# Kernel tuning notes

Measured on AMD Instinct MI355X. Metric: run time of the kernel, lower is better.

The kernel has to match this reference:

```python
import jax, jax.numpy as jnp
import numpy as np

N_NODES = 50000
N_EDGES = 1000000
N_GRAPHS = 256
ORIG = 92
ATOM = 64
NBR = 41
EPS = 1e-5


def _bn_train(h, gamma, beta):
    # BatchNorm1d in training mode: batch stats, biased variance
    mu = h.mean(axis=0)
    var = jnp.var(h, axis=0)
    return (h - mu) * jax.lax.rsqrt(var + EPS) * gamma + beta


def setup_inputs() -> dict:
    key = jax.random.key(0)
    ks = jax.random.split(key, 16)
    inp = {
        "x": jax.random.normal(ks[0], (N_NODES, ORIG), dtype=jnp.float32),
        "edge_attr": jax.random.normal(ks[1], (N_EDGES, NBR), dtype=jnp.float32),
        "lower_f": jax.random.normal(ks[2], (N_NODES, ATOM), dtype=jnp.float32),
        "edge_index": jax.random.randint(ks[3], (2, N_EDGES), 0, N_NODES, dtype=jnp.int32),
        "batch": jnp.sort(jax.random.randint(ks[4], (N_NODES,), 0, N_GRAPHS, dtype=jnp.int32)),
        # params
        "emb_W": jax.random.normal(ks[5], (ORIG, ATOM), dtype=jnp.float32) / np.sqrt(ORIG),
        "emb_b": jnp.zeros((ATOM,), dtype=jnp.float32),
        "fc_W": jax.random.normal(ks[6], (2 * ATOM + NBR, 2 * ATOM), dtype=jnp.float32) / np.sqrt(2 * ATOM + NBR),
        "fc_b": jnp.zeros((2 * ATOM,), dtype=jnp.float32),
        "bn1_g": jnp.ones((2 * ATOM,), dtype=jnp.float32),
        "bn1_b": jnp.zeros((2 * ATOM,), dtype=jnp.float32),
        "bn2_g": jnp.ones((ATOM,), dtype=jnp.float32),
        "bn2_b": jnp.zeros((ATOM,), dtype=jnp.float32),
        "att_W": jax.random.normal(ks[7], (ATOM, 1), dtype=jnp.float32) / np.sqrt(ATOM),
        "att_b": jnp.zeros((1,), dtype=jnp.float32),
        "out_W": jax.random.normal(ks[8], (ATOM, 1), dtype=jnp.float32) / np.sqrt(ATOM),
        "out_b": jnp.zeros((1,), dtype=jnp.float32),
    }
    return inp


def reference(x, edge_attr, lower_f, emb_W, emb_b, fc_W, fc_b, bn1_g, bn1_b,
              bn2_g, bn2_b, att_W, att_b, out_W, out_b, edge_index, batch):
    # embedding + lower-level features
    atom_fea = x @ emb_W + emb_b + lower_f  # [N, ATOM]

    # CGConv: gather endpoints, concat with edge features
    src, dst = edge_index[0], edge_index[1]
    total = jnp.concatenate([atom_fea[src], atom_fea[dst], edge_attr], axis=-1)  # [E, 2A+NBR]
    gated = _bn_train(total @ fc_W + fc_b, bn1_g, bn1_b)  # [E, 2A]
    nbr_filter, nbr_core = gated[:, :ATOM], gated[:, ATOM:]
    msg = jax.nn.sigmoid(nbr_filter) * jax.nn.softplus(nbr_core)  # [E, A]
    summed = jax.ops.segment_sum(msg, src, num_segments=N_NODES)  # [N, A]
    atom_out = _bn_train(summed, bn2_g, bn2_b)

    # SiLU + attentional aggregation per graph
    h = jax.nn.silu(atom_out)  # [N, A]
    logits = (h @ att_W + att_b)[:, 0]  # [N]
    seg_max = jax.ops.segment_max(logits, batch, num_segments=N_GRAPHS)
    e = jnp.exp(logits - seg_max[batch])
    denom = jax.ops.segment_sum(e, batch, num_segments=N_GRAPHS)
    alpha = e / denom[batch]  # [N]
    crys = jax.ops.segment_sum(alpha[:, None] * h, batch, num_segments=N_GRAPHS)  # [G, A]
    crys_fea = crys @ out_W + out_b  # [G, 1]
    return atom_out, crys_fea
```

## Files before the change

kernel.cpp:

```cpp
#include <hip/hip_runtime.h>
#include <math.h>

#define NN 50000
#define NE 1000000
#define NG 256
#define ORIGD 92
#define NBRD 41
#define NSPREAD 32
#define SCAN_B 256

typedef unsigned short u16;
typedef __attribute__((ext_vector_type(8))) short short8;
typedef __attribute__((ext_vector_type(4))) float f32x4;
typedef __attribute__((ext_vector_type(8))) float f32x8;

#define OFF_AFB     0
#define OFF_SUMMED  1600000
#define OFF_WT      4800000
#define OFF_BN1SPR  4812288
#define OFF_BN1SC   4820480
#define OFF_BN2ACC  4820736
#define OFF_BN2SC   4820864
#define OFF_ELOG    4820992
#define OFF_SEGMAX  4870992
#define OFF_DENOM   4871248
#define OFF_CNT     4871504
#define OFF_PTR     4921504
#define OFF_HEAD    4971504
#define OFF_BSUM    5021504
#define OFF_BOFS    5021760
#define OFF_EIDX    5022016
#define OFF_H       6022016
#define OFF_T2_END  70022016
#define OFF_P       70022016
#define OFF_T3_END  82822016
#define OFF_SRCC    82822016
#define OFF_DSTC    83822016
#define OFF_EAB     84822016
#define OFF_T4_END  108822016

__device__ __forceinline__ u16 f2b(float f) {
    unsigned u = __float_as_uint(f);
    return (u16)((u + 0x7FFFu + ((u >> 16) & 1u)) >> 16);
}
__device__ __forceinline__ float b2f(u16 u) {
    return __uint_as_float(((unsigned)u) << 16);
}
__device__ __forceinline__ float gate(float f, float cc) {
    float sig = __builtin_amdgcn_rcpf(1.f + __expf(-f));
    float sp  = fmaxf(cc, 0.f) + __logf(1.f + __expf(-fabsf(cc)));
    return sig * sp;
}
__device__ __forceinline__ float fsilu(float x) {
    return x * __builtin_amdgcn_rcpf(1.f + __expf(-x));
}

__global__ __launch_bounds__(256) void k_embed2(
    const float* __restrict__ x, const float* __restrict__ lf,
    const float* __restrict__ W, const float* __restrict__ b,
    u16* __restrict__ afb, const float* __restrict__ fcW,
    u16* __restrict__ wT3, u16* __restrict__ wP, float* __restrict__ ws)
{
    int gid = blockIdx.x * 256 + threadIdx.x;
    int n = gid >> 6, c = gid & 63;
    const float* xr = x + (long)n * ORIGD;
    float acc = b[c] + lf[gid];
#pragma unroll 4
    for (int k = 0; k < ORIGD; k++)
        acc = fmaf(xr[k], W[k * 64 + c], acc);
    afb[gid] = f2b(acc);

    if (blockIdx.x < 96) {
        int i = blockIdx.x * 256 + threadIdx.x;
        if (i < 8192) {
            int j = i >> 6, k = i & 63;
            wT3[i] = (k < NBRD) ? f2b(fcW[(128 + k) * 128 + j]) : (u16)0;
        } else {
            int i2 = i - 8192;
            int j = i2 >> 6, k = i2 & 63;
            int row = (j < 128) ? k : (64 + k);
            wP[i2] = f2b(fcW[row * 128 + (j & 127)]);
        }
    } else if (blockIdx.x < 336) {
        int zid = (blockIdx.x - 96) * 256 + threadIdx.x;
        if (zid < 8704) {
            ws[OFF_BN1SPR + zid] = 0.f;
        } else {
            int z2 = zid - 8704;
            if (z2 < 50512) ws[OFF_SEGMAX + z2] = 0.f;
        }
    }
}

__global__ void k_prepw(const float* __restrict__ fcW, u16* __restrict__ wT)
{
    int i = blockIdx.x * 256 + threadIdx.x;
    int j = i / 192, k = i - j * 192;
    wT[i] = (k < 169) ? f2b(fcW[k * 128 + j]) : (u16)0;
}

__global__ void k_prepw2(const float* __restrict__ fcW, u16* __restrict__ wT3,
                         u16* __restrict__ wP)
{
    int i = blockIdx.x * 256 + threadIdx.x;
    if (i < 8192) {
        int j = i >> 6, k = i & 63;
        wT3[i] = (k < NBRD) ? f2b(fcW[(128 + k) * 128 + j]) : (u16)0;
    } else {
        int i2 = i - 8192;
        int j = i2 >> 6, k = i2 & 63;
        int row = (j < 128) ? k : (64 + k);
        wP[i2] = f2b(fcW[row * 128 + (j & 127)]);
    }
}

__global__ __launch_bounds__(256) void k_embed(
    const float* __restrict__ x, const float* __restrict__ lf,
    const float* __restrict__ W, const float* __restrict__ b,
    u16* __restrict__ afb)
{
    int gid = blockIdx.x * 256 + threadIdx.x;
    int n = gid >> 6, c = gid & 63;
    const float* xr = x + (long)n * ORIGD;
    float acc = b[c] + lf[gid];
#pragma unroll 4
    for (int k = 0; k < ORIGD; k++)
        acc = fmaf(xr[k], W[k * 64 + c], acc);
    afb[gid] = f2b(acc);
}

template <int PACKED>
__global__ __launch_bounds__(256) void k_pnode(
    const u16* __restrict__ afb, const u16* __restrict__ wP, float* __restrict__ P)
{
    __shared__ __align__(16) u16 sB[64 * 72];
    const int tid = threadIdx.x;
    const int n0 = blockIdx.x * 64;

    for (int i = tid; i < 512; i += 256) {
        int r = i >> 3, c = i & 7;
        int n = n0 + r;
        short8 v = {0,0,0,0,0,0,0,0};
        if (n < NN) v = *(const short8*)(afb + (long)n * 64 + c * 8);
        *(short8*)(sB + r * 72 + c * 8) = v;
    }
    __syncthreads();

    const int lane = tid & 63, w = tid >> 6;
    const int n16 = lane & 15, quad = lane >> 4;
    short8 A[4][2];
#pragma unroll
    for (int m = 0; m < 4; m++) {
        const u16* base = wP + (16 * (w + 4 * m) + n16) * 64 + quad * 8;
        A[m][0] = *(const short8*)(base);
        A[m][1] = *(const short8*)(base + 32);
    }
    for (int t = 0; t < 4; t++) {
        const u16* row = sB + (16 * t + n16) * 72 + quad * 8;
        short8 b0 = *(const short8*)(row);
        short8 b1 = *(const short8*)(row + 32);
        int n = n0 + 16 * t + n16;
#pragma unroll
        for (int m = 0; m < 4; m++) {
            f32x4 acc = {0.f, 0.f, 0.f, 0.f};
            acc = __builtin_amdgcn_mfma_f32_16x16x32_bf16(A[m][0], b0, acc, 0, 0, 0);
            acc = __builtin_amdgcn_mfma_f32_16x16x32_bf16(A[m][1], b1, acc, 0, 0, 0);
            if (n < NN) {
                int M = w + 4 * m;
                int j;
                if (PACKED) {
                    int MM = M & 7;
                    j = ((M >> 3) * 128) + ((MM & 3) * 4 + quad) * 8 + ((MM >> 2) << 2);
                } else {
                    j = 16 * M + 4 * quad;
                }
                *(f32x4*)(P + (long)n * 256 + j) = acc;
            }
        }
    }
}

__global__ void k_hist(const int* __restrict__ ei, int* __restrict__ cnt)
{
    int e = blockIdx.x * 256 + threadIdx.x;
    if (e < NE) atomicAdd(&cnt[ei[e]], 1);
}

__global__ __launch_bounds__(256) void k_hist2(
    const int* __restrict__ ei, const float* __restrict__ ea,
    int* __restrict__ cnt, u16* __restrict__ eaB)
{
    long gid = (long)blockIdx.x * 256 + threadIdx.x;
    if (gid >= (long)NE * 6) return;
    int e = (int)(gid / 6);
    int q = (int)(gid - (long)e * 6);
    if (q == 0) atomicAdd(&cnt[ei[e]], 1);
    const float* row = ea + (long)e * NBRD;
    int c0 = q * 8;
    short8 v;
#pragma unroll
    for (int j = 0; j < 8; j++) {
        int c = c0 + j;
        v[j] = (c < NBRD) ? (short)f2b(row[c]) : (short)0;
    }
    *(short8*)(eaB + (long)e * 48 + c0) = v;
}

__global__ void k_partial(const int* __restrict__ cnt, int* __restrict__ lofs,
                          int* __restrict__ bsum)
{
    __shared__ int sd[SCAN_B];
    int t = threadIdx.x, b = blockIdx.x, n = b * SCAN_B + t;
    int v = (n < NN) ? cnt[n] : 0;
    sd[t] = v; __syncthreads();
    for (int o = 1; o < SCAN_B; o <<= 1) {
        int x = (t >= o) ? sd[t - o] : 0;
        __syncthreads();
        sd[t] += x;
        __syncthreads();
    }
    if (n < NN) lofs[n] = sd[t] - v;
    if (t == SCAN_B - 1) bsum[b] = sd[t];
}

__global__ void k_scanb(const int* __restrict__ bsum, int* __restrict__ bofs, int nb)
{
    __shared__ int sd[256];
    int t = threadIdx.x;
    int v = (t < nb) ? bsum[t] : 0;
    sd[t] = v; __syncthreads();
    for (int o = 1; o < 256; o <<= 1) {
        int x = (t >= o) ? sd[t - o] : 0;
        __syncthreads();
        sd[t] += x;
        __syncthreads();
    }
    bofs[t] = sd[t] - v;
}

__global__ void k_addofs(int* __restrict__ ptr, const int* __restrict__ bofs,
                         int* __restrict__ head)
{
    int n = blockIdx.x * 256 + threadIdx.x;
    if (n < NN) {
        int p = ptr[n] + bofs[n >> 8];
        ptr[n] = p; head[n] = p;
    }
}

__global__ void k_fill(const int* __restrict__ ei, int* __restrict__ head,
                       int* __restrict__ eidx)
{
    int e = blockIdx.x * 256 + threadIdx.x;
    if (e < NE) {
        int pos = atomicAdd(&head[ei[e]], 1);
        eidx[pos] = e;
    }
}

__global__ void k_fill2(const int* __restrict__ ei, int* __restrict__ head,
                        int* __restrict__ eidx, int* __restrict__ srcC,
                        int* __restrict__ dstC)
{
    int e = blockIdx.x * 256 + threadIdx.x;
    if (e < NE) {
        int s = ei[e];
        int pos = atomicAdd(&head[s], 1);
        eidx[pos] = e;
        srcC[pos] = s;
        dstC[pos] = ei[NE + e];
    }
}

__global__ __launch_bounds__(256, 4) void k_gemm_h5(
    const u16* __restrict__ eaB, const int* __restrict__ eidx,
    const int* __restrict__ srcC, const int* __restrict__ dstC,
    const u16* __restrict__ wT3, const float* __restrict__ P,
    u16* __restrict__ h, float* __restrict__ spread)
{
    const int tid = threadIdx.x;
    const int e0 = blockIdx.x * 64;
    const int lane = tid & 63, w = tid >> 6;
    const int n16 = lane & 15, quad = lane >> 4;

    short8 A0[2], A1[2];
    {
        const u16* a0 = wT3 + (16 * w + n16) * 64 + quad * 8;
        const u16* a1 = wT3 + (16 * (w + 4) + n16) * 64 + quad * 8;
        A0[0] = *(const short8*)(a0);  A0[1] = *(const short8*)(a0 + 32);
        A1[0] = *(const short8*)(a1);  A1[1] = *(const short8*)(a1 + 32);
    }

    const int j0 = 16 * w + 4 * quad;
    const int pofs = (w * 4 + quad) * 8;
    const short8 bz = {0,0,0,0,0,0,0,0};
    float s0[4] = {0,0,0,0}, q0[4] = {0,0,0,0}, s1[4] = {0,0,0,0}, q1[4] = {0,0,0,0};

    short8 b0A, b1A, b0B, b1B;
    f32x8 gSA, gDA, gSB, gDB;

#define LOADT(t, b0v, b1v, gSv, gDv)                                       \
    {                                                                      \
        int p_ = e0 + 16 * (t) + n16;                                      \
        int s_ = srcC[p_], d_ = dstC[p_], e_ = eidx[p_];                   \
        const u16* er_ = eaB + (long)e_ * 48;                              \
        b0v = *(const short8*)(er_ + quad * 8);                            \
        b1v = (quad < 2) ? *(const short8*)(er_ + 32 + quad * 8) : bz;     \
        gSv = *(const f32x8*)(P + (long)s_ * 256 + pofs);                  \
        gDv = *(const f32x8*)(P + (long)d_ * 256 + 128 + pofs);            \
    }

#define COMPT(t, b0v, b1v, gSv, gDv)                                       \
    {                                                                      \
        f32x4 acc0 = {0.f,0.f,0.f,0.f}, acc1 = {0.f,0.f,0.f,0.f};          \
        acc0 = __builtin_amdgcn_mfma_f32_16x16x32_bf16(A0[0], b0v, acc0, 0, 0, 0); \
        acc0 = __builtin_amdgcn_mfma_f32_16x16x32_bf16(A0[1], b1v, acc0, 0, 0, 0); \
        acc1 = __builtin_amdgcn_mfma_f32_16x16x32_bf16(A1[0], b0v, acc1, 0, 0, 0); \
        acc1 = __builtin_amdgcn_mfma_f32_16x16x32_bf16(A1[1], b1v, acc1, 0, 0, 0); \
        u16 hv0[4], hv1[4];                                                \
        _Pragma("unroll")                                                  \
        for (int r = 0; r < 4; r++) {                                      \
            float u0 = acc0[r] + gSv[r] + gDv[r];                          \
            float u1 = acc1[r] + gSv[4 + r] + gDv[4 + r];                  \
            s0[r] += u0; q0[r] = fmaf(u0, u0, q0[r]);                      \
            s1[r] += u1; q1[r] = fmaf(u1, u1, q1[r]);                      \
            hv0[r] = f2b(u0); hv1[r] = f2b(u1);                            \
        }                                                                  \
        u16* hp = h + (long)(e0 + 16 * (t) + n16) * 128 + j0;              \
        ushort4 v0 = make_ushort4(hv0[0], hv0[1], hv0[2], hv0[3]);         \
        ushort4 v1 = make_ushort4(hv1[0], hv1[1], hv1[2], hv1[3]);         \
        *(ushort4*)hp = v0;                                                \
        *(ushort4*)(hp + 64) = v1;                                         \
    }

    LOADT(0, b0A, b1A, gSA, gDA);
    LOADT(1, b0B, b1B, gSB, gDB);
    COMPT(0, b0A, b1A, gSA, gDA);
    LOADT(2, b0A, b1A, gSA, gDA);
    COMPT(1, b0B, b1B, gSB, gDB);
    LOADT(3, b0B, b1B, gSB, gDB);
    COMPT(2, b0A, b1A, gSA, gDA);
    COMPT(3, b0B, b1B, gSB, gDB);

#undef LOADT
#undef COMPT

#pragma unroll
    for (int m = 1; m < 16; m <<= 1) {
#pragma unroll
        for (int r = 0; r < 4; r++) {
            s0[r] += __shfl_xor(s0[r], m); q0[r] += __shfl_xor(q0[r], m);
            s1[r] += __shfl_xor(s1[r], m); q1[r] += __shfl_xor(q1[r], m);
        }
    }
    if (n16 == 0) {
        float* sp = spread + (blockIdx.x & (NSPREAD - 1)) * 256;
#pragma unroll
        for (int r = 0; r < 4; r++) {
            atomicAdd(sp + j0 + r,       s0[r]);
            atomicAdd(sp + 128 + j0 + r, q0[r]);
            atomicAdd(sp + 64 + j0 + r,  s1[r]);
            atomicAdd(sp + 192 + j0 + r, q1[r]);
        }
    }
}

__global__ __launch_bounds__(256) void k_gemm_h2(
    const float* __restrict__ ea, const int* __restrict__ ei,
    const u16* __restrict__ wT3, const float* __restrict__ P,
    u16* __restrict__ h, float* __restrict__ spread)
{
    __shared__ __align__(16) u16 sTl[64 * 72];
    __shared__ int sSrc[64], sDst[64];
    const int tid = threadIdx.x;
    const int e0 = blockIdx.x * 64;

    if (tid < 64) sSrc[tid] = ei[e0 + tid];
    else if (tid < 128) sDst[tid - 64] = ei[NE + e0 + tid - 64];

    for (int i = tid; i < 64 * 64; i += 256) {
        int e = i >> 6, c = i & 63;
        float v = (c < NBRD) ? ea[(long)(e0 + e) * NBRD + c] : 0.f;
        sTl[e * 72 + c] = f2b(v);
    }
    __syncthreads();

    const int lane = tid & 63, w = tid >> 6;
    const int n16 = lane & 15, quad = lane >> 4;

    short8 A0[2], A1[2];
    {
        const u16* b0 = wT3 + (16 * w + n16) * 64 + quad * 8;
        const u16* b1 = wT3 + (16 * (w + 4) + n16) * 64 + quad * 8;
        A0[0] = *(const short8*)(b0);  A0[1] = *(const short8*)(b0 + 32);
        A1[0] = *(const short8*)(b1);  A1[1] = *(const short8*)(b1 + 32);
    }

    const int j0 = 16 * w + 4 * quad;
    float s0[4] = {0,0,0,0}, q0[4] = {0,0,0,0}, s1[4] = {0,0,0,0}, q1[4] = {0,0,0,0};

    for (int t = 0; t < 4; t++) {
        const int ge16 = 16 * t + n16;
        const int src = sSrc[ge16], dst = sDst[ge16];
        const float* pS = P + (long)src * 256;
        const float* pD = P + (long)dst * 256 + 128;
        f32x4 g0 = *(const f32x4*)(pS + j0);
        f32x4 g1 = *(const f32x4*)(pS + 64 + j0);
        f32x4 g2 = *(const f32x4*)(pD + j0);
        f32x4 g3 = *(const f32x4*)(pD + 64 + j0);

        const u16* row = sTl + ge16 * 72 + quad * 8;
        short8 b0 = *(const short8*)(row);
        short8 b1 = *(const short8*)(row + 32);
        f32x4 acc0 = {0.f, 0.f, 0.f, 0.f}, acc1 = {0.f, 0.f, 0.f, 0.f};
        acc0 = __builtin_amdgcn_mfma_f32_16x16x32_bf16(A0[0], b0, acc0, 0, 0, 0);
        acc0 = __builtin_amdgcn_mfma_f32_16x16x32_bf16(A0[1], b1, acc0, 0, 0, 0);
        acc1 = __builtin_amdgcn_mfma_f32_16x16x32_bf16(A1[0], b0, acc1, 0, 0, 0);
        acc1 = __builtin_amdgcn_mfma_f32_16x16x32_bf16(A1[1], b1, acc1, 0, 0, 0);

        u16 hv0[4], hv1[4];
#pragma unroll
        for (int r = 0; r < 4; r++) {
            float u0 = acc0[r] + g0[r] + g2[r];
            float u1 = acc1[r] + g1[r] + g3[r];
            s0[r] += u0; q0[r] = fmaf(u0, u0, q0[r]);
            s1[r] += u1; q1[r] = fmaf(u1, u1, q1[r]);
            hv0[r] = f2b(u0); hv1[r] = f2b(u1);
        }
        int ge = e0 + ge16;
        u16* hp = h + (long)ge * 128 + j0;
        ushort4 v0 = make_ushort4(hv0[0], hv0[1], hv0[2], hv0[3]);
        ushort4 v1 = make_ushort4(hv1[0], hv1[1], hv1[2], hv1[3]);
        *(ushort4*)hp = v0;
        *(ushort4*)(hp + 64) = v1;
    }

#pragma unroll
    for (int m = 1; m < 16; m <<= 1) {
#pragma unroll
        for (int r = 0; r < 4; r++) {
            s0[r] += __shfl_xor(s0[r], m); q0[r] += __shfl_xor(q0[r], m);
            s1[r] += __shfl_xor(s1[r], m); q1[r] += __shfl_xor(q1[r], m);
        }
    }
    if (n16 == 0) {
        float* sp = spread + (blockIdx.x & (NSPREAD - 1)) * 256;
#pragma unroll
        for (int r = 0; r < 4; r++) {
            atomicAdd(sp + j0 + r,       s0[r]);
            atomicAdd(sp + 128 + j0 + r, q0[r]);
            atomicAdd(sp + 64 + j0 + r,  s1[r]);
            atomicAdd(sp + 192 + j0 + r, q1[r]);
        }
    }
}

__global__ __launch_bounds__(256) void k_gemm_h(
    const u16* __restrict__ afb, const float* __restrict__ ea,
    const int* __restrict__ ei, const u16* __restrict__ wT,
    u16* __restrict__ h, float* __restrict__ spread)
{
    __shared__ __align__(16) u16 sTl[64 * 200];
    __shared__ int sSrc[64], sDst[64];
    const int tid = threadIdx.x;
    const int e0 = blockIdx.x * 64;

    if (tid < 64) sSrc[tid] = ei[e0 + tid];
    else if (tid < 128) sDst[tid - 64] = ei[NE + e0 + tid - 64];
    __syncthreads();

    for (int i = tid; i < 1024; i += 256) {
        int e = i >> 4, q = i & 15;
        const u16* g = (q < 8) ? (afb + (long)sSrc[e] * 64 + q * 8)
                               : (afb + (long)sDst[e] * 64 + (q - 8) * 8);
        *(short8*)(sTl + e * 200 + q * 8) = *(const short8*)g;
    }
    for (int i = tid; i < 64 * 64; i += 256) {
        int e = i >> 6, c = i & 63;
        float v = (c < NBRD) ? ea[(long)(e0 + e) * NBRD + c] : 0.f;
        sTl[e * 200 + 128 + c] = f2b(v);
    }
    __syncthreads();

    const int lane = tid & 63, w = tid >> 6;
    const int n16 = lane & 15, quad = lane >> 4;

    short8 A0[6], A1[6];
    {
        const u16* b0 = wT + (16 * w + n16) * 192 + quad * 8;
        const u16* b1 = wT + (16 * (w + 4) + n16) * 192 + quad * 8;
#pragma unroll
        for (int ks = 0; ks < 6; ks++) {
            A0[ks] = *(const short8*)(b0 + ks * 32);
            A1[ks] = *(const short8*)(b1 + ks * 32);
        }
    }

    const int j0 = 16 * w + 4 * quad;
    float s0[4] = {0,0,0,0}, q0[4] = {0,0,0,0}, s1[4] = {0,0,0,0}, q1[4] = {0,0,0,0};

    for (int t = 0; t < 4; t++) {
        const u16* row = sTl + (16 * t + n16) * 200 + quad * 8;
        f32x4 acc0 = {0.f, 0.f, 0.f, 0.f}, acc1 = {0.f, 0.f, 0.f, 0.f};
#pragma unroll
        for (int ks = 0; ks < 6; ks++) {
            short8 b = *(const short8*)(row + ks * 32);
            acc0 = __builtin_amdgcn_mfma_f32_16x16x32_bf16(A0[ks], b, acc0, 0, 0, 0);
            acc1 = __builtin_amdgcn_mfma_f32_16x16x32_bf16(A1[ks], b, acc1, 0, 0, 0);
        }
#pragma unroll
        for (int r = 0; r < 4; r++) {
            s0[r] += acc0[r]; q0[r] = fmaf(acc0[r], acc0[r], q0[r]);
            s1[r] += acc1[r]; q1[r] = fmaf(acc1[r], acc1[r], q1[r]);
        }
        int ge = e0 + 16 * t + n16;
        u16* hp = h + (long)ge * 128 + j0;
        ushort4 v0 = make_ushort4(f2b(acc0[0]), f2b(acc0[1]), f2b(acc0[2]), f2b(acc0[3]));
        ushort4 v1 = make_ushort4(f2b(acc1[0]), f2b(acc1[1]), f2b(acc1[2]), f2b(acc1[3]));
        *(ushort4*)hp = v0;
        *(ushort4*)(hp + 64) = v1;
    }

#pragma unroll
    for (int m = 1; m < 16; m <<= 1) {
#pragma unroll
        for (int r = 0; r < 4; r++) {
            s0[r] += __shfl_xor(s0[r], m); q0[r] += __shfl_xor(q0[r], m);
            s1[r] += __shfl_xor(s1[r], m); q1[r] += __shfl_xor(q1[r], m);
        }
    }
    if (n16 == 0) {
        float* sp = spread + (blockIdx.x & (NSPREAD - 1)) * 256;
#pragma unroll
        for (int r = 0; r < 4; r++) {
            atomicAdd(sp + j0 + r,       s0[r]);
            atomicAdd(sp + 128 + j0 + r, q0[r]);
            atomicAdd(sp + 64 + j0 + r,  s1[r]);
            atomicAdd(sp + 192 + j0 + r, q1[r]);
        }
    }
}

template <int MODE>
__global__ __launch_bounds__(256) void k_gemm(
    const u16* __restrict__ afb, const float* __restrict__ ea,
    const int* __restrict__ ei, const u16* __restrict__ wT,
    const float* __restrict__ sc, float* __restrict__ outbuf)
{
    __shared__ __align__(16) u16 sTl[64 * 200];
    __shared__ int sSrc[64], sDst[64];
    const int tid = threadIdx.x;
    const int e0 = blockIdx.x * 64;

    if (tid < 64) sSrc[tid] = ei[e0 + tid];
    else if (tid < 128) sDst[tid - 64] = ei[NE + e0 + tid - 64];
    __syncthreads();
    for (int i = tid; i < 1024; i += 256) {
        int e = i >> 4, q = i & 15;
        const u16* g = (q < 8) ? (afb + (long)sSrc[e] * 64 + q * 8)
                               : (afb + (long)sDst[e] * 64 + (q - 8) * 8);
        *(short8*)(sTl + e * 200 + q * 8) = *(const short8*)g;
    }
    for (int i = tid; i < 64 * 64; i += 256) {
        int e = i >> 6, c = i & 63;
        float v = (c < NBRD) ? ea[(long)(e0 + e) * NBRD + c] : 0.f;
        sTl[e * 200 + 128 + c] = f2b(v);
    }
    __syncthreads();

    const int lane = tid & 63, w = tid >> 6;
    const int n16 = lane & 15, quad = lane >> 4;
    short8 A0[6], A1[6];
    {
        const u16* b0 = wT + (16 * w + n16) * 192 + quad * 8;
        const u16* b1 = wT + (16 * (w + 4) + n16) * 192 + quad * 8;
#pragma unroll
        for (int ks = 0; ks < 6; ks++) {
            A0[ks] = *(const short8*)(b0 + ks * 32);
            A1[ks] = *(const short8*)(b1 + ks * 32);
        }
    }
    const int j0 = 16 * w + 4 * quad;
    float s0[4] = {0,0,0,0}, q0[4] = {0,0,0,0}, s1[4] = {0,0,0,0}, q1[4] = {0,0,0,0};
    float scf[4], shf[4], scc[4], shc[4];
    if (MODE == 1) {
#pragma unroll
        for (int r = 0; r < 4; r++) {
            scf[r] = sc[j0 + r];        shf[r] = sc[128 + j0 + r];
            scc[r] = sc[64 + j0 + r];   shc[r] = sc[192 + j0 + r];
        }
    }
    for (int t = 0; t < 4; t++) {
        const u16* row = sTl + (16 * t + n16) * 200 + quad * 8;
        f32x4 acc0 = {0.f, 0.f, 0.f, 0.f}, acc1 = {0.f, 0.f, 0.f, 0.f};
#pragma unroll
        for (int ks = 0; ks < 6; ks++) {
            short8 b = *(const short8*)(row + ks * 32);
            acc0 = __builtin_amdgcn_mfma_f32_16x16x32_bf16(A0[ks], b, acc0, 0, 0, 0);
            acc1 = __builtin_amdgcn_mfma_f32_16x16x32_bf16(A1[ks], b, acc1, 0, 0, 0);
        }
        if (MODE == 0) {
#pragma unroll
            for (int r = 0; r < 4; r++) {
                s0[r] += acc0[r]; q0[r] = fmaf(acc0[r], acc0[r], q0[r]);
                s1[r] += acc1[r]; q1[r] = fmaf(acc1[r], acc1[r], q1[r]);
            }
        } else {
            int src = sSrc[16 * t + n16];
            float* dst = outbuf + (long)src * 64 + j0;
#pragma unroll
            for (int r = 0; r < 4; r++) {
                float f  = fmaf(acc0[r], scf[r], shf[r]);
                float cc = fmaf(acc1[r], scc[r], shc[r]);
                atomicAdd(dst + r, gate(f, cc));
            }
        }
    }
    if (MODE == 0) {
#pragma unroll
        for (int m = 1; m < 16; m <<= 1) {
#pragma unroll
            for (int r = 0; r < 4; r++) {
                s0[r] += __shfl_xor(s0[r], m); q0[r] += __shfl_xor(q0[r], m);
                s1[r] += __shfl_xor(s1[r], m); q1[r] += __shfl_xor(q1[r], m);
            }
        }
        if (n16 == 0) {
            float* sp = outbuf + (blockIdx.x & (NSPREAD - 1)) * 256;
#pragma unroll
            for (int r = 0; r < 4; r++) {
                atomicAdd(sp + j0 + r,       s0[r]);
                atomicAdd(sp + 128 + j0 + r, q0[r]);
                atomicAdd(sp + 64 + j0 + r,  s1[r]);
                atomicAdd(sp + 192 + j0 + r, q1[r]);
            }
        }
    }
}

__global__ void k_bn1fin(const float* __restrict__ spread,
                         const float* __restrict__ g, const float* __restrict__ b,
                         float* __restrict__ sc)
{
    int c = threadIdx.x;
    float s = 0.f, q = 0.f;
    for (int k = 0; k < NSPREAD; k++) { s += spread[k * 256 + c]; q += spread[k * 256 + 128 + c]; }
    float mean_acc = s / (float)NE;
    float var = q / (float)NE - mean_acc * mean_acc;
    float scale = g[c] * rsqrtf(var + 1e-5f);
    sc[c] = scale;
    sc[128 + c] = b[c] - mean_acc * scale;
}

__global__ __launch_bounds__(256) void k_scatter3(
    const u16* __restrict__ h, const int* __restrict__ ptr,
    const int* __restrict__ cnt, const float* __restrict__ spread,
    const float* __restrict__ g, const float* __restrict__ b,
    float* __restrict__ summed)
{
    __shared__ float ssc[256];
    int tid = threadIdx.x;
    if (tid < 128) {
        int c = tid;
        float s = 0.f, q = 0.f;
        for (int k = 0; k < NSPREAD; k++) {
            s += spread[k * 256 + c]; q += spread[k * 256 + 128 + c];
        }
        float mean_acc = s / (float)NE;
        float var = q / (float)NE - mean_acc * mean_acc;
        float scale = g[c] * rsqrtf(var + 1e-5f);
        ssc[c] = scale;
        ssc[128 + c] = b[c] - mean_acc * scale;
    }
    __syncthreads();

    int n = blockIdx.x * 4 + (tid >> 6);
    int l = tid & 63;
    int es = l & 7, cg = l >> 3;

    float scf[8], shf[8], scc[8], shc[8];
#pragma unroll
    for (int j = 0; j < 8; j++) {
        scf[j] = ssc[cg * 8 + j];
        shf[j] = ssc[128 + cg * 8 + j];
        scc[j] = ssc[64 + cg * 8 + j];
        shc[j] = ssc[192 + cg * 8 + j];
    }

    int p0 = ptr[n], deg = cnt[n];
    float acc[8] = {0,0,0,0,0,0,0,0};
    for (int i = 0; i < deg; i += 8) {
        int idx = i + es;
        bool valid = idx < deg;
        int row = p0 + (valid ? idx : 0);
        const u16* hr = h + (long)row * 128;
        short8 f8 = *(const short8*)(hr + cg * 8);
        short8 c8 = *(const short8*)(hr + 64 + cg * 8);
#pragma unroll
        for (int j = 0; j < 8; j++) {
            float f  = fmaf(b2f((u16)f8[j]), scf[j], shf[j]);
            float cc = fmaf(b2f((u16)c8[j]), scc[j], shc[j]);
            float gg = gate(f, cc);
            acc[j] += valid ? gg : 0.f;
        }
    }
#pragma unroll
    for (int m = 1; m < 8; m <<= 1)
#pragma unroll
        for (int j = 0; j < 8; j++) acc[j] += __shfl_xor(acc[j], m);
    if (es == 0) {
        float* sp = summed + (long)n * 64 + cg * 8;
        float4 v0 = {acc[0], acc[1], acc[2], acc[3]};
        float4 v1 = {acc[4], acc[5], acc[6], acc[7]};
        *(float4*)sp = v0;
        *(float4*)(sp + 4) = v1;
    }
}

__global__ __launch_bounds__(256) void k_scatter(
    const u16* __restrict__ h, const int* __restrict__ ptr,
    const int* __restrict__ cnt, const int* __restrict__ eidx,
    const float* __restrict__ sc, float* __restrict__ summed)
{
    int tid = threadIdx.x;
    int n = blockIdx.x * 4 + (tid >> 6);
    int l = tid & 63;
    int es = l & 7, cg = l >> 3;

    float4 a0 = *(const float4*)(sc + cg * 8);
    float4 a1 = *(const float4*)(sc + cg * 8 + 4);
    float4 b0 = *(const float4*)(sc + 128 + cg * 8);
    float4 b1 = *(const float4*)(sc + 128 + cg * 8 + 4);
    float4 c0 = *(const float4*)(sc + 64 + cg * 8);
    float4 c1 = *(const float4*)(sc + 64 + cg * 8 + 4);
    float4 d0 = *(const float4*)(sc + 192 + cg * 8);
    float4 d1 = *(const float4*)(sc + 192 + cg * 8 + 4);
    float scf[8] = {a0.x,a0.y,a0.z,a0.w,a1.x,a1.y,a1.z,a1.w};
    float shf[8] = {b0.x,b0.y,b0.z,b0.w,b1.x,b1.y,b1.z,b1.w};
    float scc[8] = {c0.x,c0.y,c0.z,c0.w,c1.x,c1.y,c1.z,c1.w};
    float shc[8] = {d0.x,d0.y,d0.z,d0.w,d1.x,d1.y,d1.z,d1.w};

    int p0 = ptr[n], deg = cnt[n];
    float acc[8] = {0,0,0,0,0,0,0,0};
    for (int i = 0; i < deg; i += 8) {
        int idx = i + es;
        bool valid = idx < deg;
        int e = eidx[p0 + (valid ? idx : 0)];
        const u16* hr = h + (long)e * 128;
        short8 f8 = *(const short8*)(hr + cg * 8);
        short8 c8 = *(const short8*)(hr + 64 + cg * 8);
#pragma unroll
        for (int j = 0; j < 8; j++) {
            float f  = fmaf(b2f((u16)f8[j]), scf[j], shf[j]);
            float cc = fmaf(b2f((u16)c8[j]), scc[j], shc[j]);
            float gg = gate(f, cc);
            acc[j] += valid ? gg : 0.f;
        }
    }
#pragma unroll
    for (int m = 1; m < 8; m <<= 1)
#pragma unroll
        for (int j = 0; j < 8; j++) acc[j] += __shfl_xor(acc[j], m);
    if (es == 0) {
        float* sp = summed + (long)n * 64 + cg * 8;
        float4 v0 = {acc[0], acc[1], acc[2], acc[3]};
        float4 v1 = {acc[4], acc[5], acc[6], acc[7]};
        *(float4*)sp = v0;
        *(float4*)(sp + 4) = v1;
    }
}

__global__ __launch_bounds__(256) void k_bn2stats(const float* __restrict__ summed,
                                                  float* __restrict__ acc2)
{
    int tid = threadIdx.x; int c = tid & 63; int sub = tid >> 6;
    float s = 0.f, q = 0.f;
    for (int r = blockIdx.x * 4 + sub; r < NN; r += 4 * 128) {
        float v = summed[(long)r * 64 + c]; s += v; q = fmaf(v, v, q);
    }
    __shared__ float rs[256], rq[256];
    rs[tid] = s; rq[tid] = q; __syncthreads();
    if (tid < 64) {
        s = rs[tid] + rs[tid + 64] + rs[tid + 128] + rs[tid + 192];
        q = rq[tid] + rq[tid + 64] + rq[tid + 128] + rq[tid + 192];
        atomicAdd(&acc2[tid], s);
        atomicAdd(&acc2[64 + tid], q);
    }
}

__global__ void k_bn2fin(const float* __restrict__ acc2,
                         const float* __restrict__ g, const float* __restrict__ b,
                         float* __restrict__ sc2, const float* __restrict__ outb,
                         float* __restrict__ out)
{
    int c = threadIdx.x;
    if (c < 64) {
        float mean = acc2[c] / (float)NN;
        float var = acc2[64 + c] / (float)NN - mean * mean;
        float scale = g[c] * rsqrtf(var + 1e-5f);
        sc2[c] = scale;
        sc2[64 + c] = b[c] - mean * scale;
    }
    out[(long)NN * 64 + c] = outb[0];
}

__global__ __launch_bounds__(256) void k_nodepost2(
    const float* __restrict__ summed, const float* __restrict__ acc2,
    const float* __restrict__ g, const float* __restrict__ b,
    const float* __restrict__ attW, const float* __restrict__ attb,
    const int* __restrict__ batch, float* __restrict__ out,
    float* __restrict__ elog, unsigned* __restrict__ segmax)
{
    __shared__ float ssc2[128];
    int tid = threadIdx.x;
    if (tid < 64) {
        float mean = acc2[tid] / (float)NN;
        float var = acc2[64 + tid] / (float)NN - mean * mean;
        float scale = g[tid] * rsqrtf(var + 1e-5f);
        ssc2[tid] = scale;
        ssc2[64 + tid] = b[tid] - mean * scale;
    }
    __syncthreads();

    int n = blockIdx.x * 4 + (tid >> 6); int c = tid & 63;
    float v = summed[(long)n * 64 + c];
    float ao = fmaf(v, ssc2[c], ssc2[64 + c]);
    out[(long)n * 64 + c] = ao;
    float h = fsilu(ao);
    float p = h * attW[c];
#pragma unroll
    for (int off = 32; off; off >>= 1) p += __shfl_down(p, off, 64);
    if (c == 0) {
        float logit = p + attb[0];
        elog[n] = logit;
        unsigned u = __float_as_uint(logit);
        u = (u & 0x80000000u) ? ~u : (u | 0x80000000u);
        atomicMax(&segmax[batch[n]], u);
    }
}

__global__ __launch_bounds__(256) void k_nodepost(
    const float* __restrict__ summed, const float* __restrict__ sc2,
    const float* __restrict__ attW, const float* __restrict__ attb,
    const int* __restrict__ batch, float* __restrict__ out,
    float* __restrict__ elog, unsigned* __restrict__ segmax)
{
    int tid = threadIdx.x; int n = blockIdx.x * 4 + (tid >> 6); int c = tid & 63;
    float v = summed[(long)n * 64 + c];
    float ao = fmaf(v, sc2[c], sc2[64 + c]);
    out[(long)n * 64 + c] = ao;
    float h = fsilu(ao);
    float p = h * attW[c];
#pragma unroll
    for (int off = 32; off; off >>= 1) p += __shfl_down(p, off, 64);
    if (c == 0) {
        float logit = p + attb[0];
        elog[n] = logit;
        unsigned u = __float_as_uint(logit);
        u = (u & 0x80000000u) ? ~u : (u | 0x80000000u);
        atomicMax(&segmax[batch[n]], u);
    }
}

__global__ void k_denom2(const int* __restrict__ batch,
                         const unsigned* __restrict__ segmax,
                         float* __restrict__ elog, float* __restrict__ denom,
                         const float* __restrict__ outb, float* __restrict__ out)
{
    int n = blockIdx.x * 256 + threadIdx.x;
    if (n < NG) out[(long)NN * 64 + n] = outb[0];
    if (n >= NN) return;
    int b = batch[n];
    unsigned u = segmax[b];
    u = (u & 0x80000000u) ? (u & 0x7FFFFFFFu) : ~u;
    float e = __expf(elog[n] - __uint_as_float(u));
    elog[n] = e;
    atomicAdd(&denom[b], e);
}

__global__ void k_denom(const int* __restrict__ batch,
                        const unsigned* __restrict__ segmax,
                        float* __restrict__ elog, float* __restrict__ denom)
{
    int n = blockIdx.x * 256 + threadIdx.x;
    if (n >= NN) return;
    int b = batch[n];
    unsigned u = segmax[b];
    u = (u & 0x80000000u) ? (u & 0x7FFFFFFFu) : ~u;
    float e = __expf(elog[n] - __uint_as_float(u));
    elog[n] = e;
    atomicAdd(&denom[b], e);
}

__global__ __launch_bounds__(256) void k_crys(
    const float* __restrict__ atom_out, const float* __restrict__ elog,
    const float* __restrict__ denom, const int* __restrict__ batch,
    const float* __restrict__ outW, float* __restrict__ out)
{
    int tid = threadIdx.x; int n = blockIdx.x * 4 + (tid >> 6); int l = tid & 63;
    int b = batch[n];
    float alpha = elog[n] / denom[b];
    float ao = atom_out[(long)n * 64 + l];
    float p = fsilu(ao) * outW[l];
#pragma unroll
    for (int off = 32; off; off >>= 1) p += __shfl_down(p, off, 64);
    if (l == 0) atomicAdd(&out[(long)NN * 64 + b], alpha * p);
}

extern "C" void kernel_launch(void* const* d_in, const int* in_sizes, int n_in,
                              void* d_out, int out_size, void* d_ws, size_t ws_size,
                              hipStream_t stream)
{
    const float* x    = (const float*)d_in[0];
    const float* eatt = (const float*)d_in[1];
    const float* lf   = (const float*)d_in[2];
    const int*   ei   = (const int*)d_in[3];
    const int*   batch= (const int*)d_in[4];
    const float* embW = (const float*)d_in[5];
    const float* embB = (const float*)d_in[6];
    const float* fcW  = (const float*)d_in[7];
    const float* bn1g = (const float*)d_in[9];
    const float* bn1b = (const float*)d_in[10];
    const float* bn2g = (const float*)d_in[11];
    const float* bn2b = (const float*)d_in[12];
    const float* attW = (const float*)d_in[13];
    const float* attB = (const float*)d_in[14];
    const float* outW = (const float*)d_in[15];
    const float* outB = (const float*)d_in[16];
    float* out = (float*)d_out;
    float* ws  = (float*)d_ws;

    u16* afb  = (u16*)(ws + OFF_AFB);
    u16* wT   = (u16*)(ws + OFF_WT);
    int* cnt  = (int*)(ws + OFF_CNT);
    int* ptr  = (int*)(ws + OFF_PTR);
    int* head = (int*)(ws + OFF_HEAD);
    int* bsum = (int*)(ws + OFF_BSUM);
    int* bofs = (int*)(ws + OFF_BOFS);
    int* eidx = (int*)(ws + OFF_EIDX);
    u16* h    = (u16*)(ws + OFF_H);

    const bool t4 = ws_size >= (size_t)OFF_T4_END * sizeof(float);
    const bool t3 = ws_size >= (size_t)OFF_T3_END * sizeof(float);
    const bool t2 = ws_size >= (size_t)OFF_T2_END * sizeof(float);

    if (t4) {
        u16* wT3  = wT;
        u16* wP   = wT + 8192;
        float* P  = ws + OFF_P;
        int* srcC = (int*)(ws + OFF_SRCC);
        int* dstC = (int*)(ws + OFF_DSTC);
        u16* eaB  = (u16*)(ws + OFF_EAB);
        k_embed2<<<12500, 256, 0, stream>>>(x, lf, embW, embB, afb, fcW, wT3, wP, ws);
        k_hist2<<<(NE * 6 + 255) / 256, 256, 0, stream>>>(ei, eatt, cnt, eaB);
        k_partial<<<(NN + SCAN_B - 1) / SCAN_B, SCAN_B, 0, stream>>>(cnt, ptr, bsum);
        k_scanb<<<1, 256, 0, stream>>>(bsum, bofs, (NN + SCAN_B - 1) / SCAN_B);
        k_addofs<<<(NN + 255) / 256, 256, 0, stream>>>(ptr, bofs, head);
        k_fill2<<<(NE + 255) / 256, 256, 0, stream>>>(ei, head, eidx, srcC, dstC);
        k_pnode<1><<<(NN + 63) / 64, 256, 0, stream>>>(afb, wP, P);
        k_gemm_h5<<<NE / 64, 256, 0, stream>>>(eaB, eidx, srcC, dstC, wT3, P, h,
                                               ws + OFF_BN1SPR);
        k_scatter3<<<NN / 4, 256, 0, stream>>>(h, ptr, cnt, ws + OFF_BN1SPR,
                                               bn1g, bn1b, ws + OFF_SUMMED);
        k_bn2stats<<<128, 256, 0, stream>>>(ws + OFF_SUMMED, ws + OFF_BN2ACC);
        k_nodepost2<<<12500, 256, 0, stream>>>(ws + OFF_SUMMED, ws + OFF_BN2ACC,
                                               bn2g, bn2b, attW, attB, batch, out,
                                               ws + OFF_ELOG,
                                               (unsigned*)(ws + OFF_SEGMAX));
        k_denom2<<<196, 256, 0, stream>>>(batch, (const unsigned*)(ws + OFF_SEGMAX),
                                          ws + OFF_ELOG, ws + OFF_DENOM, outB, out);
        k_crys<<<12500, 256, 0, stream>>>(out, ws + OFF_ELOG, ws + OFF_DENOM, batch,
                                          outW, out);
        return;
    }

    k_embed<<<12500, 256, 0, stream>>>(x, lf, embW, embB, afb);

    if (t3) {
        u16* wT3 = wT;
        u16* wP  = wT + 8192;
        float* P = ws + OFF_P;
        k_prepw2<<<96, 256, 0, stream>>>(fcW, wT3, wP);
        hipMemsetAsync(ws + OFF_BN1SPR, 0,
                       (size_t)(OFF_PTR - OFF_BN1SPR) * sizeof(float), stream);
        k_hist<<<(NE + 255) / 256, 256, 0, stream>>>(ei, cnt);
        k_partial<<<(NN + SCAN_B - 1) / SCAN_B, SCAN_B, 0, stream>>>(cnt, ptr, bsum);
        k_scanb<<<1, 256, 0, stream>>>(bsum, bofs, (NN + SCAN_B - 1) / SCAN_B);
        k_addofs<<<(NN + 255) / 256, 256, 0, stream>>>(ptr, bofs, head);
        k_fill<<<(NE + 255) / 256, 256, 0, stream>>>(ei, head, eidx);
        k_pnode<0><<<(NN + 63) / 64, 256, 0, stream>>>(afb, wP, P);
        k_gemm_h2<<<NE / 64, 256, 0, stream>>>(eatt, ei, wT3, P, h, ws + OFF_BN1SPR);
        k_bn1fin<<<1, 128, 0, stream>>>(ws + OFF_BN1SPR, bn1g, bn1b, ws + OFF_BN1SC);
        k_scatter<<<NN / 4, 256, 0, stream>>>(h, ptr, cnt, eidx, ws + OFF_BN1SC,
                                              ws + OFF_SUMMED);
    } else if (t2) {
        k_prepw<<<96, 256, 0, stream>>>(fcW, wT);
        hipMemsetAsync(ws + OFF_BN1SPR, 0,
                       (size_t)(OFF_PTR - OFF_BN1SPR) * sizeof(float), stream);
        k_hist<<<(NE + 255) / 256, 256, 0, stream>>>(ei, cnt);
        k_partial<<<(NN + SCAN_B - 1) / SCAN_B, SCAN_B, 0, stream>>>(cnt, ptr, bsum);
        k_scanb<<<1, 256, 0, stream>>>(bsum, bofs, (NN + SCAN_B - 1) / SCAN_B);
        k_addofs<<<(NN + 255) / 256, 256, 0, stream>>>(ptr, bofs, head);
        k_fill<<<(NE + 255) / 256, 256, 0, stream>>>(ei, head, eidx);
        k_gemm_h<<<NE / 64, 256, 0, stream>>>(afb, eatt, ei, wT, h, ws + OFF_BN1SPR);
        k_bn1fin<<<1, 128, 0, stream>>>(ws + OFF_BN1SPR, bn1g, bn1b, ws + OFF_BN1SC);
        k_scatter<<<NN / 4, 256, 0, stream>>>(h, ptr, cnt, eidx, ws + OFF_BN1SC,
                                              ws + OFF_SUMMED);
    } else {
        k_prepw<<<96, 256, 0, stream>>>(fcW, wT);
        hipMemsetAsync(ws + OFF_SUMMED, 0,
                       (size_t)(OFF_PTR - OFF_SUMMED) * sizeof(float), stream);
        k_gemm<0><<<NE / 64, 256, 0, stream>>>(afb, eatt, ei, wT, ws + OFF_BN1SC,
                                               ws + OFF_BN1SPR);
        k_bn1fin<<<1, 128, 0, stream>>>(ws + OFF_BN1SPR, bn1g, bn1b, ws + OFF_BN1SC);
        k_gemm<1><<<NE / 64, 256, 0, stream>>>(afb, eatt, ei, wT, ws + OFF_BN1SC,
                                               ws + OFF_SUMMED);
    }

    k_bn2stats<<<128, 256, 0, stream>>>(ws + OFF_SUMMED, ws + OFF_BN2ACC);
    k_bn2fin<<<1, 256, 0, stream>>>(ws + OFF_BN2ACC, bn2g, bn2b, ws + OFF_BN2SC,
                                    outB, out);
    k_nodepost<<<12500, 256, 0, stream>>>(ws + OFF_SUMMED, ws + OFF_BN2SC, attW, attB,
                                          batch, out, ws + OFF_ELOG,
                                          (unsigned*)(ws + OFF_SEGMAX));
    k_denom<<<196, 256, 0, stream>>>(batch, (const unsigned*)(ws + OFF_SEGMAX),
                                     ws + OFF_ELOG, ws + OFF_DENOM);
    k_crys<<<12500, 256, 0, stream>>>(out, ws + OFF_ELOG, ws + OFF_DENOM, batch,
                                      outW, out);
}
```

Before: 1.194 ms.

## Split node projections into fp32 src and bf16 dst tables, interleave h layout

```diff
diff --git a/kernel.cpp b/kernel.cpp
--- a/kernel.cpp
+++ b/kernel.cpp
@@ -33,6 +33,7 @@
 #define OFF_H       6022016
 #define OFF_T2_END  70022016
 #define OFF_P       70022016
+#define OFF_P2      76422016
 #define OFF_T3_END  82822016
 #define OFF_SRCC    82822016
 #define OFF_DSTC    83822016
@@ -129,7 +130,6 @@
     afb[gid] = f2b(acc);
 }
 
-template <int PACKED>
 __global__ __launch_bounds__(256) void k_pnode(
     const u16* __restrict__ afb, const u16* __restrict__ wP, float* __restrict__ P)
 {
@@ -166,15 +166,60 @@
             acc = __builtin_amdgcn_mfma_f32_16x16x32_bf16(A[m][0], b0, acc, 0, 0, 0);
             acc = __builtin_amdgcn_mfma_f32_16x16x32_bf16(A[m][1], b1, acc, 0, 0, 0);
             if (n < NN) {
+                int j = 16 * (w + 4 * m) + 4 * quad;
+                *(f32x4*)(P + (long)n * 256 + j) = acc;
+            }
+        }
+    }
+}
+
+__global__ __launch_bounds__(256) void k_pnodeS(
+    const u16* __restrict__ afb, const u16* __restrict__ wP,
+    float* __restrict__ P1, u16* __restrict__ P2)
+{
+    __shared__ __align__(16) u16 sB[64 * 72];
+    const int tid = threadIdx.x;
+    const int n0 = blockIdx.x * 64;
+
+    for (int i = tid; i < 512; i += 256) {
+        int r = i >> 3, c = i & 7;
+        int n = n0 + r;
+        short8 v = {0,0,0,0,0,0,0,0};
+        if (n < NN) v = *(const short8*)(afb + (long)n * 64 + c * 8);
+        *(short8*)(sB + r * 72 + c * 8) = v;
+    }
+    __syncthreads();
+
+    const int lane = tid & 63, w = tid >> 6;
+    const int n16 = lane & 15, quad = lane >> 4;
+    short8 A[4][2];
+#pragma unroll
+    for (int m = 0; m < 4; m++) {
+        const u16* base = wP + (16 * (w + 4 * m) + n16) * 64 + quad * 8;
+        A[m][0] = *(const short8*)(base);
+        A[m][1] = *(const short8*)(base + 32);
+    }
+    for (int t = 0; t < 4; t++) {
+        const u16* row = sB + (16 * t + n16) * 72 + quad * 8;
+        short8 b0 = *(const short8*)(row);
+        short8 b1 = *(const short8*)(row + 32);
+        int n = n0 + 16 * t + n16;
+#pragma unroll
+        for (int m = 0; m < 4; m++) {
+            f32x4 acc = {0.f, 0.f, 0.f, 0.f};
+            acc = __builtin_amdgcn_mfma_f32_16x16x32_bf16(A[m][0], b0, acc, 0, 0, 0);
+            acc = __builtin_amdgcn_mfma_f32_16x16x32_bf16(A[m][1], b1, acc, 0, 0, 0);
+            if (n < NN) {
                 int M = w + 4 * m;
-                int j;
-                if (PACKED) {
-                    int MM = M & 7;
-                    j = ((M >> 3) * 128) + ((MM & 3) * 4 + quad) * 8 + ((MM >> 2) << 2);
+                int MM = M & 7;
+                int inner = ((MM & 3) * 4 + quad) * 8 + ((MM >> 2) << 2);
+                if (M < 8) {
+                    *(f32x4*)(P1 + (long)n * 128 + inner) = acc;
                 } else {
-                    j = 16 * M + 4 * quad;
+                    ushort4 v = make_ushort4(f2b(acc[0]), f2b(acc[1]),
+                                             f2b(acc[2]), f2b(acc[3]));
+                    *(ushort4*)(P2 + (long)n * 128 + inner) = v;
                 }
-                *(f32x4*)(P + (long)n * 256 + j) = acc;
             }
         }
     }
@@ -272,11 +317,12 @@
     }
 }
 
-__global__ __launch_bounds__(256, 4) void k_gemm_h5(
+__global__ __launch_bounds__(256) void k_gemm_h6(
     const u16* __restrict__ eaB, const int* __restrict__ eidx,
     const int* __restrict__ srcC, const int* __restrict__ dstC,
-    const u16* __restrict__ wT3, const float* __restrict__ P,
-    u16* __restrict__ h, float* __restrict__ spread)
+    const u16* __restrict__ wT3, const float* __restrict__ P1,
+    const u16* __restrict__ P2, u16* __restrict__ h,
+    float* __restrict__ spread)
 {
     const int tid = threadIdx.x;
     const int e0 = blockIdx.x * 64;
@@ -296,54 +342,42 @@
     const short8 bz = {0,0,0,0,0,0,0,0};
     float s0[4] = {0,0,0,0}, q0[4] = {0,0,0,0}, s1[4] = {0,0,0,0}, q1[4] = {0,0,0,0};
 
-    short8 b0A, b1A, b0B, b1B;
-    f32x8 gSA, gDA, gSB, gDB;
-
-#define LOADT(t, b0v, b1v, gSv, gDv)                                       \
-    {                                                                      \
-        int p_ = e0 + 16 * (t) + n16;                                      \
-        int s_ = srcC[p_], d_ = dstC[p_], e_ = eidx[p_];                   \
-        const u16* er_ = eaB + (long)e_ * 48;                              \
-        b0v = *(const short8*)(er_ + quad * 8);                            \
-        b1v = (quad < 2) ? *(const short8*)(er_ + 32 + quad * 8) : bz;     \
-        gSv = *(const f32x8*)(P + (long)s_ * 256 + pofs);                  \
-        gDv = *(const f32x8*)(P + (long)d_ * 256 + 128 + pofs);            \
-    }
-
-#define COMPT(t, b0v, b1v, gSv, gDv)                                       \
-    {                                                                      \
-        f32x4 acc0 = {0.f,0.f,0.f,0.f}, acc1 = {0.f,0.f,0.f,0.f};          \
-        acc0 = __builtin_amdgcn_mfma_f32_16x16x32_bf16(A0[0], b0v, acc0, 0, 0, 0); \
-        acc0 = __builtin_amdgcn_mfma_f32_16x16x32_bf16(A0[1], b1v, acc0, 0, 0, 0); \
-        acc1 = __builtin_amdgcn_mfma_f32_16x16x32_bf16(A1[0], b0v, acc1, 0, 0, 0); \
-        acc1 = __builtin_amdgcn_mfma_f32_16x16x32_bf16(A1[1], b1v, acc1, 0, 0, 0); \
-        u16 hv0[4], hv1[4];                                                \
-        _Pragma("unroll")                                                  \
-        for (int r = 0; r < 4; r++) {                                      \
-            float u0 = acc0[r] + gSv[r] + gDv[r];                          \
-            float u1 = acc1[r] + gSv[4 + r] + gDv[4 + r];                  \
-            s0[r] += u0; q0[r] = fmaf(u0, u0, q0[r]);                      \
-            s1[r] += u1; q1[r] = fmaf(u1, u1, q1[r]);                      \
-            hv0[r] = f2b(u0); hv1[r] = f2b(u1);                            \
-        }                                                                  \
-        u16* hp = h + (long)(e0 + 16 * (t) + n16) * 128 + j0;              \
-        ushort4 v0 = make_ushort4(hv0[0], hv0[1], hv0[2], hv0[3]);         \
-        ushort4 v1 = make_ushort4(hv1[0], hv1[1], hv1[2], hv1[3]);         \
-        *(ushort4*)hp = v0;                                                \
-        *(ushort4*)(hp + 64) = v1;                                         \
-    }
-
-    LOADT(0, b0A, b1A, gSA, gDA);
-    LOADT(1, b0B, b1B, gSB, gDB);
-    COMPT(0, b0A, b1A, gSA, gDA);
-    LOADT(2, b0A, b1A, gSA, gDA);
-    COMPT(1, b0B, b1B, gSB, gDB);
-    LOADT(3, b0B, b1B, gSB, gDB);
-    COMPT(2, b0A, b1A, gSA, gDA);
-    COMPT(3, b0B, b1B, gSB, gDB);
-
-#undef LOADT
-#undef COMPT
+#pragma unroll
+    for (int t = 0; t < 4; t++) {
+        const int pos = e0 + 16 * t + n16;
+        const int src = srcC[pos];
+        const int dst = dstC[pos];
+        const int e   = eidx[pos];
+
+        const u16* er = eaB + (long)e * 48;
+        short8 b0 = *(const short8*)(er + quad * 8);
+        short8 b1 = (quad < 2) ? *(const short8*)(er + 32 + quad * 8) : bz;
+
+        f32x8 gS = *(const f32x8*)(P1 + (long)src * 128 + pofs);
+        short8 gDb = *(const short8*)(P2 + (long)dst * 128 + pofs);
+
+        f32x4 acc0 = {0.f, 0.f, 0.f, 0.f}, acc1 = {0.f, 0.f, 0.f, 0.f};
+        acc0 = __builtin_amdgcn_mfma_f32_16x16x32_bf16(A0[0], b0, acc0, 0, 0, 0);
+        acc0 = __builtin_amdgcn_mfma_f32_16x16x32_bf16(A0[1], b1, acc0, 0, 0, 0);
+        acc1 = __builtin_amdgcn_mfma_f32_16x16x32_bf16(A1[0], b0, acc1, 0, 0, 0);
+        acc1 = __builtin_amdgcn_mfma_f32_16x16x32_bf16(A1[1], b1, acc1, 0, 0, 0);
+
+        u16 hv0[4], hv1[4];
+#pragma unroll
+        for (int r = 0; r < 4; r++) {
+            float u0 = acc0[r] + gS[r]     + b2f((u16)gDb[r]);
+            float u1 = acc1[r] + gS[4 + r] + b2f((u16)gDb[4 + r]);
+            s0[r] += u0; q0[r] = fmaf(u0, u0, q0[r]);
+            s1[r] += u1; q1[r] = fmaf(u1, u1, q1[r]);
+            hv0[r] = f2b(u0); hv1[r] = f2b(u1);
+        }
+        short8 hv;
+        hv[0] = (short)hv0[0]; hv[1] = (short)hv1[0];
+        hv[2] = (short)hv0[1]; hv[3] = (short)hv1[1];
+        hv[4] = (short)hv0[2]; hv[5] = (short)hv1[2];
+        hv[6] = (short)hv0[3]; hv[7] = (short)hv1[3];
+        *(short8*)(h + (long)pos * 128 + j0 * 2) = hv;
+    }
 
 #pragma unroll
     for (int m = 1; m < 16; m <<= 1) {
@@ -652,7 +686,7 @@
     sc[128 + c] = b[c] - mean_acc * scale;
 }
 
-__global__ __launch_bounds__(256) void k_scatter3(
+__global__ __launch_bounds__(256) void k_scatter4(
     const u16* __restrict__ h, const int* __restrict__ ptr,
     const int* __restrict__ cnt, const float* __restrict__ spread,
     const float* __restrict__ g, const float* __restrict__ b,
@@ -693,15 +727,22 @@
         int idx = i + es;
         bool valid = idx < deg;
         int row = p0 + (valid ? idx : 0);
-        const u16* hr = h + (long)row * 128;
-        short8 f8 = *(const short8*)(hr + cg * 8);
-        short8 c8 = *(const short8*)(hr + 64 + cg * 8);
-#pragma unroll
-        for (int j = 0; j < 8; j++) {
-            float f  = fmaf(b2f((u16)f8[j]), scf[j], shf[j]);
-            float cc = fmaf(b2f((u16)c8[j]), scc[j], shc[j]);
+        const u16* hr = h + (long)row * 128 + cg * 16;
+        short8 A = *(const short8*)(hr);
+        short8 B = *(const short8*)(hr + 8);
+#pragma unroll
+        for (int j = 0; j < 4; j++) {
+            float f  = fmaf(b2f((u16)A[2 * j]),     scf[j], shf[j]);
+            float cc = fmaf(b2f((u16)A[2 * j + 1]), scc[j], shc[j]);
             float gg = gate(f, cc);
             acc[j] += valid ? gg : 0.f;
+        }
+#pragma unroll
+        for (int j = 0; j < 4; j++) {
+            float f  = fmaf(b2f((u16)B[2 * j]),     scf[4 + j], shf[4 + j]);
+            float cc = fmaf(b2f((u16)B[2 * j + 1]), scc[4 + j], shc[4 + j]);
+            float gg = gate(f, cc);
+            acc[4 + j] += valid ? gg : 0.f;
         }
     }
 #pragma unroll
@@ -947,7 +988,8 @@
     if (t4) {
         u16* wT3  = wT;
         u16* wP   = wT + 8192;
-        float* P  = ws + OFF_P;
+        float* P1 = ws + OFF_P;
+        u16* P2   = (u16*)(ws + OFF_P2);
         int* srcC = (int*)(ws + OFF_SRCC);
         int* dstC = (int*)(ws + OFF_DSTC);
         u16* eaB  = (u16*)(ws + OFF_EAB);
@@ -957,10 +999,10 @@
         k_scanb<<<1, 256, 0, stream>>>(bsum, bofs, (NN + SCAN_B - 1) / SCAN_B);
         k_addofs<<<(NN + 255) / 256, 256, 0, stream>>>(ptr, bofs, head);
         k_fill2<<<(NE + 255) / 256, 256, 0, stream>>>(ei, head, eidx, srcC, dstC);
-        k_pnode<1><<<(NN + 63) / 64, 256, 0, stream>>>(afb, wP, P);
-        k_gemm_h5<<<NE / 64, 256, 0, stream>>>(eaB, eidx, srcC, dstC, wT3, P, h,
+        k_pnodeS<<<(NN + 63) / 64, 256, 0, stream>>>(afb, wP, P1, P2);
+        k_gemm_h6<<<NE / 64, 256, 0, stream>>>(eaB, eidx, srcC, dstC, wT3, P1, P2, h,
                                                ws + OFF_BN1SPR);
-        k_scatter3<<<NN / 4, 256, 0, stream>>>(h, ptr, cnt, ws + OFF_BN1SPR,
+        k_scatter4<<<NN / 4, 256, 0, stream>>>(h, ptr, cnt, ws + OFF_BN1SPR,
                                                bn1g, bn1b, ws + OFF_SUMMED);
         k_bn2stats<<<128, 256, 0, stream>>>(ws + OFF_SUMMED, ws + OFF_BN2ACC);
         k_nodepost2<<<12500, 256, 0, stream>>>(ws + OFF_SUMMED, ws + OFF_BN2ACC,
@@ -988,7 +1030,7 @@
         k_scanb<<<1, 256, 0, stream>>>(bsum, bofs, (NN + SCAN_B - 1) / SCAN_B);
         k_addofs<<<(NN + 255) / 256, 256, 0, stream>>>(ptr, bofs, head);
         k_fill<<<(NE + 255) / 256, 256, 0, stream>>>(ei, head, eidx);
-        k_pnode<0><<<(NN + 63) / 64, 256, 0, stream>>>(afb, wP, P);
+        k_pnode<<<(NN + 63) / 64, 256, 0, stream>>>(afb, wP, P);
         k_gemm_h2<<<NE / 64, 256, 0, stream>>>(eatt, ei, wT3, P, h, ws + OFF_BN1SPR);
         k_bn1fin<<<1, 128, 0, stream>>>(ws + OFF_BN1SPR, bn1g, bn1b, ws + OFF_BN1SC);
         k_scatter<<<NN / 4, 256, 0, stream>>>(h, ptr, cnt, eidx, ws + OFF_BN1SC,
```

New measurement: 1.155 ms. 1.03x faster.
